# Kernel optimization log

Hardware: AMD Instinct MI355X
Metric: run time of the kernel (lower is better)

The kernel has to match this reference:

```python
import jax, jax.numpy as jnp
import numpy as np

HIDDEN = 768
NUM_HEADS = 8
NUM_CELLS = 16384
MAX_HDRS = 8
NUM_HEADERS = 512
LN_EPS = 1e-5


def setup_inputs() -> dict:
    key = jax.random.key(0)
    ks = jax.random.split(key, 16)
    s = 0.02
    D = HIDDEN
    return {
        "cell_value_embeddings": jax.random.normal(ks[0], (NUM_CELLS, D), jnp.float32),
        "header_embeddings": jax.random.normal(ks[1], (NUM_HEADERS, D), jnp.float32),
        "cell_to_header_map": jax.random.randint(ks[2], (NUM_CELLS, MAX_HDRS), 0, NUM_HEADERS),
        "cell_positions": jax.random.randint(ks[3], (NUM_CELLS, 2), 0, 100),
        # nn.MultiheadAttention params
        "in_proj_w": jax.random.normal(ks[4], (3 * D, D), jnp.float32) * s,
        "in_proj_b": jnp.zeros((3 * D,), jnp.float32),
        "out_w": jax.random.normal(ks[5], (D, D), jnp.float32) * s,
        "out_b": jnp.zeros((D,), jnp.float32),
        # positional embedding tables
        "row_emb": jax.random.normal(ks[6], (100, D), jnp.float32) * s,
        "col_emb": jax.random.normal(ks[7], (100, D), jnp.float32) * s,
        # fusion: Linear(2D->D) + LayerNorm
        "fus_w": jax.random.normal(ks[8], (D, 2 * D), jnp.float32) * s,
        "fus_b": jnp.zeros((D,), jnp.float32),
        "ln_g": jnp.ones((D,), jnp.float32),
        "ln_b": jnp.zeros((D,), jnp.float32),
    }


def _forward(cell_value_embeddings, header_embeddings, in_proj_w, in_proj_b,
             out_w, out_b, row_emb, col_emb, fus_w, fus_b, ln_g, ln_b,
             cell_to_header_map, cell_positions):
    N, D = cell_value_embeddings.shape
    H = cell_to_header_map.shape[1]
    nh, dh = NUM_HEADS, D // NUM_HEADS
    scale = 1.0 / (dh ** 0.5)

    pos = jnp.clip(cell_positions, 0, 99)
    cwp = cell_value_embeddings + row_emb[pos[:, 0]] + col_emb[pos[:, 1]]  # [N,D]

    ids = cell_to_header_map
    mask = ids >= 0                                   # [N,H] valid header slots
    hg = header_embeddings[jnp.where(mask, ids, 0)]   # [N,H,D] gathered K/V inputs

    Wq, Wk, Wv = jnp.split(in_proj_w, 3, axis=0)
    bq, bk, bv = jnp.split(in_proj_b, 3)
    q = (cwp @ Wq.T + bq).reshape(N, nh, dh)          # [N,a,d]
    k = (hg @ Wk.T + bk).reshape(N, H, nh, dh)        # [N,k,a,d]
    v = (hg @ Wv.T + bv).reshape(N, H, nh, dh)

    scores = jnp.einsum('nad,nkad->nak', q, k) * scale          # [N,a,k]
    scores = jnp.where(mask[:, None, :], scores, -1e9)
    attn = jax.nn.softmax(scores, axis=-1)
    attn = jnp.where(mask[:, None, :], attn, 0.0)
    ctx = jnp.einsum('nak,nkad->nad', attn, v).reshape(N, D)
    att_out = ctx @ out_w.T + out_b                    # [N,D]

    comb = jnp.concatenate([cwp, att_out], axis=-1)    # [N,2D]
    h = comb @ fus_w.T + fus_b
    mu = jnp.mean(h, axis=-1, keepdims=True)
    var = jnp.mean((h - mu) ** 2, axis=-1, keepdims=True)
    h = (h - mu) * jax.lax.rsqrt(var + LN_EPS) * ln_g + ln_b
    fused = jax.nn.relu(h)

    has = jnp.any(mask, axis=-1)                       # cells with >=1 valid header
    enriched = jnp.where(has[:, None], fused, cwp)
    weights = jnp.where(mask, attn.mean(axis=1), 0.0)  # head-averaged attn [N,H]
    return enriched, weights


def reference(cell_value_embeddings, header_embeddings, cell_to_header_map,
              cell_positions, in_proj_w, in_proj_b, out_w, out_b, row_emb,
              col_emb, fus_w, fus_b, ln_g, ln_b):
    return _forward(cell_value_embeddings, header_embeddings, in_proj_w,
                    in_proj_b, out_w, out_b, row_emb, col_emb, fus_w, fus_b,
                    ln_g, ln_b, cell_to_header_map, cell_positions)
```

## Files before the change

### kernel.cpp

```cpp
#include <hip/hip_runtime.h>
#include <hip/hip_bf16.h>

#define NCELLS 16384
#define DIM    768
#define NHEADS 8
#define DHEAD  96
#define MAXH   8
#define ND     (NCELLS * DIM)


using bf16 = __hip_bfloat16;
typedef short  short8  __attribute__((ext_vector_type(8)));
typedef short  short4v __attribute__((ext_vector_type(4)));
typedef float  floatx4 __attribute__((ext_vector_type(4)));

__device__ inline short f2b(float f) {
    bf16 h = __float2bfloat16(f);
    unsigned short u; __builtin_memcpy(&u, &h, 2); return (short)u;
}
__device__ inline float b2f(short u) {
    unsigned x = ((unsigned)(unsigned short)u) << 16;
    float f; __builtin_memcpy(&f, &x, 4); return f;
}

__device__ inline short8 ld8(const float* p) {
    floatx4 a = *reinterpret_cast<const floatx4*>(p);
    floatx4 b = *reinterpret_cast<const floatx4*>(p + 4);
    short8 o;
#pragma unroll
    for (int i = 0; i < 4; ++i) { o[i] = f2b(a[i]); o[i + 4] = f2b(b[i]); }
    return o;
}

__device__ __forceinline__ void cp16(const void* g, void* l) {
    __builtin_amdgcn_global_load_lds(
        (const __attribute__((address_space(1))) void*)g,
        (__attribute__((address_space(3))) void*)l, 16, 0, 0);
}

template <int DUAL, int COUT>
__global__ __launch_bounds__(256) void gemm_bf(
    const bf16* __restrict__ A, const bf16* __restrict__ A2,
    const bf16* __restrict__ W, int ldw,
    const float* __restrict__ bias,
    float* __restrict__ Cf, bf16* __restrict__ Cb, int K)
{
    __shared__ short As[128 * 64];
    __shared__ short Bs[128 * 64];
    const int tid = threadIdx.x, wave = tid >> 6, lane = tid & 63;
    const int id = blockIdx.x;
    const int m0 = (id & 127) * 128;
    const int n0 = (id >> 7) * 128;
    const int wr = (wave & 1) * 64, wc = (wave >> 1) * 64;
    const int fr = lane & 15, kg = lane >> 4;

    const int srow = lane >> 3;
    const int scol = (lane & 7) ^ srow;

    floatx4 acc[16];
#pragma unroll
    for (int i = 0; i < 16; ++i) acc[i] = (floatx4){0.f, 0.f, 0.f, 0.f};

    for (int k0 = 0; k0 < K; k0 += 64) {
        const bf16* Ak; int ka;
        if (!DUAL || k0 < DIM) { Ak = A;  ka = k0; }
        else                   { Ak = A2; ka = k0 - DIM; }

        __syncthreads();
#pragma unroll
        for (int i = 0; i < 4; ++i) {
            const int c = i * 4 + wave;
            const int row = c * 8 + srow;
            cp16(Ak + (size_t)(m0 + row) * DIM + ka + scol * 8,
                 &As[c * 512 + lane * 8]);
            cp16(W  + (size_t)(n0 + row) * ldw + k0 + scol * 8,
                 &Bs[c * 512 + lane * 8]);
        }
        __syncthreads();

#pragma unroll
        for (int kk = 0; kk < 2; ++kk) {
            short8 af[4], bfv[4];
#pragma unroll
            for (int i = 0; i < 4; ++i) {
                const int sa = ((kk * 4 + kg) ^ (fr & 7)) * 8;
                af[i]  = *reinterpret_cast<const short8*>(&As[(wr + i * 16 + fr) * 64 + sa]);
                bfv[i] = *reinterpret_cast<const short8*>(&Bs[(wc + i * 16 + fr) * 64 + sa]);
            }
#pragma unroll
            for (int i = 0; i < 4; ++i)
#pragma unroll
                for (int j = 0; j < 4; ++j)
                    acc[i * 4 + j] = __builtin_amdgcn_mfma_f32_16x16x32_bf16(
                        af[i], bfv[j], acc[i * 4 + j], 0, 0, 0);
        }
    }

    const int col_l = lane & 15, row_q = kg * 4;
#pragma unroll
    for (int j = 0; j < 4; ++j) {
        const int col = n0 + wc + j * 16 + col_l;
        const float bv = bias[col];
#pragma unroll
        for (int i = 0; i < 4; ++i) {
#pragma unroll
            for (int r = 0; r < 4; ++r) {
                const int row = m0 + wr + i * 16 + row_q + r;
                const float v = acc[i * 4 + j][r] + bv;
                if (COUT == 0) Cf[(size_t)row * DIM + col] = v;
                else           Cb[(size_t)row * DIM + col] = __float2bfloat16(v);
            }
        }
    }
}

__global__ __launch_bounds__(512) void gemm_ln_kernel(
    const bf16* __restrict__ A, const bf16* __restrict__ A2,
    const bf16* __restrict__ W,
    const float* __restrict__ bco, float* __restrict__ out,
    const int* __restrict__ map,
    const float* __restrict__ ce, const int* __restrict__ pos,
    const float* __restrict__ re, const float* __restrict__ co,
    const float* __restrict__ g, const float* __restrict__ b)
{
    __shared__ short As[8 * 512];
    __shared__ short Bs[32 * 512];
    __shared__ float rsum[64][4], rsq[64][4];
    __shared__ int   hasf[64];

    const int tid = threadIdx.x, wave = tid >> 6, lane = tid & 63;
    const int m0 = blockIdx.x * 64;
    const int wr = (wave & 1) * 32, wc = (wave >> 1) * 64;
    const int fr = lane & 15, kg = lane >> 4;
    const int srow = lane >> 3;
    const int scol = (lane & 7) ^ srow;
    const int col_l = lane & 15, rq = kg * 4;

    if (tid < 256) { ((float*)rsum)[tid] = 0.f; ((float*)rsq)[tid] = 0.f; }
    if (tid < 64) hasf[tid] = 0;

    for (int nt = 0; nt < 3; ++nt) {
        const int n0b = nt * 256;
        floatx4 acc[8];
#pragma unroll
        for (int i = 0; i < 8; ++i) acc[i] = (floatx4){0.f, 0.f, 0.f, 0.f};

        for (int k0 = 0; k0 < 1536; k0 += 64) {
            const bf16* Ak; int ka;
            if (k0 < DIM) { Ak = A;  ka = k0; }
            else          { Ak = A2; ka = k0 - DIM; }

            __syncthreads();
            cp16(Ak + (size_t)(m0 + wave * 8 + srow) * DIM + ka + scol * 8,
                 &As[wave * 512 + lane * 8]);
#pragma unroll
            for (int u = 0; u < 4; ++u) {
                const int c2 = wave * 4 + u;
                cp16(W + (size_t)(n0b + c2 * 8 + srow) * 1536 + k0 + scol * 8,
                     &Bs[c2 * 512 + lane * 8]);
            }
            __syncthreads();

#pragma unroll
            for (int kk = 0; kk < 2; ++kk) {
                const int sa = ((kk * 4 + kg) ^ (fr & 7)) * 8;
                short8 af[2], bv[4];
#pragma unroll
                for (int i = 0; i < 2; ++i)
                    af[i] = *reinterpret_cast<const short8*>(&As[(wr + i * 16 + fr) * 64 + sa]);
#pragma unroll
                for (int j = 0; j < 4; ++j)
                    bv[j] = *reinterpret_cast<const short8*>(&Bs[(wc + j * 16 + fr) * 64 + sa]);
#pragma unroll
                for (int i = 0; i < 2; ++i)
#pragma unroll
                    for (int j = 0; j < 4; ++j)
                        acc[i * 4 + j] = __builtin_amdgcn_mfma_f32_16x16x32_bf16(
                            af[i], bv[j], acc[i * 4 + j], 0, 0, 0);
            }
        }

        float bcov[4];
#pragma unroll
        for (int j = 0; j < 4; ++j) bcov[j] = bco[n0b + wc + j * 16 + col_l];
#pragma unroll
        for (int i = 0; i < 2; ++i) {
#pragma unroll
            for (int r = 0; r < 4; ++r) {
                const int rowl = wr + i * 16 + rq + r;
                float s = 0.f, q = 0.f;
#pragma unroll
                for (int j = 0; j < 4; ++j) {
                    const int col = n0b + wc + j * 16 + col_l;
                    const float v = acc[i * 4 + j][r] + bcov[j];
                    out[(size_t)(m0 + rowl) * DIM + col] = v;
                    s += v; q += v * v;
                }
#pragma unroll
                for (int off = 1; off < 16; off <<= 1) {
                    s += __shfl_xor(s, off);
                    q += __shfl_xor(q, off);
                }
                if (col_l == 0) {
                    rsum[rowl][wave >> 1] += s;
                    rsq[rowl][wave >> 1]  += q;
                }
            }
        }
    }

    {
        const int row = tid >> 3, sl = tid & 7;
        if (map[(size_t)(m0 + row) * MAXH + sl] >= 0) hasf[row] = 1;
    }
    __syncthreads();

    {
        const int rowl = tid >> 3, c0 = (tid & 7) * 96;
        const int grow = m0 + rowl;
        const float sr = rsum[rowl][0] + rsum[rowl][1] + rsum[rowl][2] + rsum[rowl][3];
        const float qr = rsq[rowl][0] + rsq[rowl][1] + rsq[rowl][2] + rsq[rowl][3];
        const float mu  = sr * (1.f / 768.f);
        const float var = qr * (1.f / 768.f) - mu * mu;
        const float inv = rsqrtf(var + 1e-5f);
        float* hp = out + (size_t)grow * DIM + c0;

        if (hasf[rowl]) {
#pragma unroll 4
            for (int bq = 0; bq < 24; ++bq) {
                floatx4 hv = *reinterpret_cast<const floatx4*>(hp + bq * 4);
                floatx4 gv = *reinterpret_cast<const floatx4*>(g + c0 + bq * 4);
                floatx4 bv = *reinterpret_cast<const floatx4*>(b + c0 + bq * 4);
                floatx4 o;
#pragma unroll
                for (int e = 0; e < 4; ++e)
                    o[e] = fmaxf((hv[e] - mu) * inv * gv[e] + bv[e], 0.f);
                *reinterpret_cast<floatx4*>(hp + bq * 4) = o;
            }
        } else {
            int pr = pos[grow * 2 + 0]; pr = min(max(pr, 0), 99);
            int pc = pos[grow * 2 + 1]; pc = min(max(pc, 0), 99);
#pragma unroll 4
            for (int bq = 0; bq < 24; ++bq) {
                floatx4 a0 = *reinterpret_cast<const floatx4*>(ce + (size_t)grow * DIM + c0 + bq * 4);
                floatx4 b0 = *reinterpret_cast<const floatx4*>(re + (size_t)pr * DIM + c0 + bq * 4);
                floatx4 c1 = *reinterpret_cast<const floatx4*>(co + (size_t)pc * DIM + c0 + bq * 4);
                floatx4 o;
#pragma unroll
                for (int e = 0; e < 4; ++e) o[e] = a0[e] + b0[e] + c1[e];
                *reinterpret_cast<floatx4*>(hp + bq * 4) = o;
            }
        }
    }
}

__global__ __launch_bounds__(256) void prep_kernel(
    const float* __restrict__ ce, const int* __restrict__ pos,
    const float* __restrict__ re, const float* __restrict__ co,
    bf16* __restrict__ cwp_b,
    const float* __restrict__ in_proj_w, bf16* __restrict__ Wq_b,
    const float* __restrict__ fus_w,     bf16* __restrict__ Wf_b,
    const float* __restrict__ out_w, const float* __restrict__ out_b,
    const float* __restrict__ fus_b, float* __restrict__ bco,
    const float* __restrict__ hdr, const float* __restrict__ in_proj_b,
    bf16* __restrict__ HKV)
{
    __shared__ short As[64 * 72];
    __shared__ short Bs[64 * 72];
    const int b = blockIdx.x, tid = threadIdx.x;

    if (b < 192) {
        const int m0 = (b & 7) * 64, n0 = (b >> 3) * 64;
        const float* W = in_proj_w + (size_t)DIM * DIM;
        const float* bias = in_proj_b + DIM;
        const int wave = tid >> 6, lane = tid & 63;
        const int lr = tid >> 2, lc = (tid & 3) * 16;
        const int fr = lane & 15, fk = (lane >> 4) * 8;

        floatx4 acc[4];
#pragma unroll
        for (int i = 0; i < 4; ++i) acc[i] = (floatx4){0.f, 0.f, 0.f, 0.f};

        const float* ap = hdr + (size_t)(m0 + lr) * DIM + lc;
        const float* wp = W   + (size_t)(n0 + lr) * DIM + lc;
        short8 a0 = ld8(ap), a1 = ld8(ap + 8);
        short8 w0 = ld8(wp), w1 = ld8(wp + 8);

        for (int it = 0; it < 12; ++it) {
            __syncthreads();
            *reinterpret_cast<short8*>(&As[lr * 72 + lc])     = a0;
            *reinterpret_cast<short8*>(&As[lr * 72 + lc + 8]) = a1;
            *reinterpret_cast<short8*>(&Bs[lr * 72 + lc])     = w0;
            *reinterpret_cast<short8*>(&Bs[lr * 72 + lc + 8]) = w1;
            __syncthreads();
            if (it < 11) {
                const int k0 = (it + 1) * 64;
                a0 = ld8(ap + k0); a1 = ld8(ap + k0 + 8);
                w0 = ld8(wp + k0); w1 = ld8(wp + k0 + 8);
            }
#pragma unroll
            for (int kk = 0; kk < 2; ++kk) {
                short8 af = *reinterpret_cast<const short8*>(
                    &As[(wave * 16 + fr) * 72 + kk * 32 + fk]);
#pragma unroll
                for (int t = 0; t < 4; ++t) {
                    short8 bfv = *reinterpret_cast<const short8*>(
                        &Bs[(t * 16 + fr) * 72 + kk * 32 + fk]);
                    acc[t] = __builtin_amdgcn_mfma_f32_16x16x32_bf16(af, bfv, acc[t], 0, 0, 0);
                }
            }
        }
        const int col_l = lane & 15, row_q = (lane >> 4) * 4;
#pragma unroll
        for (int t = 0; t < 4; ++t) {
            const int col = n0 + t * 16 + col_l;
            const float bv = bias[col];
#pragma unroll
            for (int r = 0; r < 4; ++r) {
                const int row = m0 + wave * 16 + row_q + r;
                HKV[(size_t)row * 1536 + col] = __float2bfloat16(acc[t][r] + bv);
            }
        }
    } else if (b < 336) {
        const int b3 = b - 192;
        const int n0  = (b3 % 12) * 64;
        const int k0t = (b3 / 12) * 64;
        const int wave = tid >> 6, lane = tid & 63;
        const int lr = tid >> 2, lc = (tid & 3) * 16;
        const int fr = lane & 15, fk = (lane >> 4) * 8;

        floatx4 acc[4];
#pragma unroll
        for (int i = 0; i < 4; ++i) acc[i] = (floatx4){0.f, 0.f, 0.f, 0.f};

        const float* ap = fus_w + (size_t)(n0 + lr) * 1536 + 768 + lc;
        const float* bp = out_w + (size_t)lr * DIM + k0t + lc;
        short8 a0 = ld8(ap), a1 = ld8(ap + 8);
        floatx4 q0 = *reinterpret_cast<const floatx4*>(bp);
        floatx4 q1 = *reinterpret_cast<const floatx4*>(bp + 4);
        floatx4 q2 = *reinterpret_cast<const floatx4*>(bp + 8);
        floatx4 q3 = *reinterpret_cast<const floatx4*>(bp + 12);

        for (int it = 0; it < 12; ++it) {
            __syncthreads();
            *reinterpret_cast<short8*>(&As[lr * 72 + lc])     = a0;
            *reinterpret_cast<short8*>(&As[lr * 72 + lc + 8]) = a1;
#pragma unroll
            for (int e = 0; e < 4; ++e) {
                Bs[(lc + e) * 72 + lr]      = f2b(q0[e]);
                Bs[(lc + 4 + e) * 72 + lr]  = f2b(q1[e]);
                Bs[(lc + 8 + e) * 72 + lr]  = f2b(q2[e]);
                Bs[(lc + 12 + e) * 72 + lr] = f2b(q3[e]);
            }
            __syncthreads();
            if (it < 11) {
                const int r0 = (it + 1) * 64;
                a0 = ld8(ap + r0); a1 = ld8(ap + r0 + 8);
                const float* bq = bp + (size_t)r0 * DIM;
                q0 = *reinterpret_cast<const floatx4*>(bq);
                q1 = *reinterpret_cast<const floatx4*>(bq + 4);
                q2 = *reinterpret_cast<const floatx4*>(bq + 8);
                q3 = *reinterpret_cast<const floatx4*>(bq + 12);
            }
#pragma unroll
            for (int kk = 0; kk < 2; ++kk) {
                short8 af = *reinterpret_cast<const short8*>(
                    &As[(wave * 16 + fr) * 72 + kk * 32 + fk]);
#pragma unroll
                for (int t = 0; t < 4; ++t) {
                    short8 bfv = *reinterpret_cast<const short8*>(
                        &Bs[(t * 16 + fr) * 72 + kk * 32 + fk]);
                    acc[t] = __builtin_amdgcn_mfma_f32_16x16x32_bf16(af, bfv, acc[t], 0, 0, 0);
                }
            }
        }
        const int col_l = lane & 15, row_q = (lane >> 4) * 4;
#pragma unroll
        for (int t = 0; t < 4; ++t) {
            const int col = k0t + t * 16 + col_l;
#pragma unroll
            for (int r = 0; r < 4; ++r) {
                const int row = n0 + wave * 16 + row_q + r;
                Wf_b[(size_t)row * 1536 + 768 + col] = __float2bfloat16(acc[t][r]);
            }
        }
    } else if (b < 339) {
        const int n = (b - 336) * 256 + tid;
        const float* wrow = fus_w + (size_t)n * 1536 + 768;
        float acc = fus_b[n];
#pragma unroll 4
        for (int m = 0; m < 768; m += 4) {
            floatx4 wv = *reinterpret_cast<const floatx4*>(wrow + m);
            floatx4 ob = *reinterpret_cast<const floatx4*>(out_b + m);
            acc += wv[0] * ob[0] + wv[1] * ob[1] + wv[2] * ob[2] + wv[3] * ob[3];
        }
        bco[n] = acc;
    } else if (b < 915) {
        const int i = (b - 339) * 256 + tid;
        floatx4 v = *reinterpret_cast<const floatx4*>(in_proj_w + (size_t)i * 4);
        short4v o;
#pragma unroll
        for (int j = 0; j < 4; ++j) o[j] = f2b(v[j]);
        *reinterpret_cast<short4v*>((short*)Wq_b + (size_t)i * 4) = o;
    } else if (b < 1491) {
        const int i  = (b - 915) * 256 + tid;
        const int e0 = i * 4;
        const int n  = e0 / 768;
        const int k  = e0 - n * 768;
        const size_t src = (size_t)n * 1536 + k;
        floatx4 v = *reinterpret_cast<const floatx4*>(fus_w + src);
        short4v o;
#pragma unroll
        for (int j = 0; j < 4; ++j) o[j] = f2b(v[j]);
        *reinterpret_cast<short4v*>((short*)Wf_b + src) = o;
    } else {
        const int gid  = (b - 1491) * 256 + tid;
        const int cell = gid / 96;
        const int off  = (gid % 96) * 8;
        int pr = pos[cell * 2 + 0]; pr = min(max(pr, 0), 99);
        int pc = pos[cell * 2 + 1]; pc = min(max(pc, 0), 99);
        const float* a = ce + (size_t)cell * DIM + off;
        const float* bb = re + (size_t)pr * DIM + off;
        const float* c = co + (size_t)pc * DIM + off;
        floatx4 a0 = *reinterpret_cast<const floatx4*>(a);
        floatx4 a1 = *reinterpret_cast<const floatx4*>(a + 4);
        floatx4 b0 = *reinterpret_cast<const floatx4*>(bb);
        floatx4 b1 = *reinterpret_cast<const floatx4*>(bb + 4);
        floatx4 c0 = *reinterpret_cast<const floatx4*>(c);
        floatx4 c1 = *reinterpret_cast<const floatx4*>(c + 4);
        short8 o;
#pragma unroll
        for (int i = 0; i < 4; ++i) {
            o[i]     = f2b(a0[i] + b0[i] + c0[i]);
            o[i + 4] = f2b(a1[i] + b1[i] + c1[i]);
        }
        *reinterpret_cast<short8*>((short*)cwp_b + (size_t)cell * DIM + off) = o;
    }
}

__global__ __launch_bounds__(256) void attn_l_kernel(
    const bf16* __restrict__ q, bf16* __restrict__ ctx,
    const bf16* __restrict__ HKV, const int* __restrict__ map,
    float* __restrict__ wout)
{
    const int h = threadIdx.x >> 7;
    const int t = threadIdx.x & 127;
    const int cell = blockIdx.x * 2 + h;

    __shared__ short Ks[2][8 * 768];
    __shared__ int   ids[2][MAXH];
    __shared__ float msk[2][MAXH];
    __shared__ float at_l[2][64];

    if (t < MAXH) {
        int id = map[(size_t)cell * MAXH + t];
        msk[h][t] = (id >= 0) ? 1.f : 0.f;
        ids[h][t] = (id >= 0) ? id : 0;
    }

    const int a = t >> 3, j = t & 7;
    short8 qv[12];
    if (t < 64) {
        const short* qp = (const short*)q + (size_t)cell * DIM + a * DHEAD;
#pragma unroll
        for (int c = 0; c < 12; ++c)
            qv[c] = *reinterpret_cast<const short8*>(qp + c * 8);
    }

#pragma unroll
    for (int s = 0; s < 6; ++s) {
        const int P  = s * 128 + t;
        const int jr = P / 96;
        const int gi = (P - jr * 96) ^ (jr & 7);
        int id = map[(size_t)cell * MAXH + jr];
        id = (id >= 0) ? id : 0;
        cp16((const short*)HKV + (size_t)id * 1536 + gi * 8, &Ks[h][P * 8]);
    }
    __syncthreads();

    short8 vv[8];
    if (t < 96) {
        const int d0 = t * 8;
#pragma unroll
        for (int jj = 0; jj < 8; ++jj)
            vv[jj] = *reinterpret_cast<const short8*>(
                (const short*)HKV + (size_t)ids[h][jj] * 1536 + DIM + d0);
    }

    if (t < 64) {
        float s0 = 0.f, s1 = 0.f, s2 = 0.f, s3 = 0.f;
#pragma unroll
        for (int cc = 0; cc < 12; cc += 4) {
            short8 kv[4];
#pragma unroll
            for (int u = 0; u < 4; ++u) {
                const int gi = (a * 12 + cc + u) ^ (j & 7);
                kv[u] = *reinterpret_cast<const short8*>(&Ks[h][(j * 96 + gi) * 8]);
            }
#pragma unroll
            for (int e = 0; e < 8; ++e) {
                s0 += b2f(qv[cc    ][e]) * b2f(kv[0][e]);
                s1 += b2f(qv[cc + 1][e]) * b2f(kv[1][e]);
                s2 += b2f(qv[cc + 2][e]) * b2f(kv[2][e]);
                s3 += b2f(qv[cc + 3][e]) * b2f(kv[3][e]);
            }
        }
        float s = ((s0 + s1) + (s2 + s3)) * 0.10206207261596577f;
        const float mk = msk[h][j];
        s = (mk != 0.f) ? s : -1e9f;
        float m = s;
        m = fmaxf(m, __shfl_xor(m, 1));
        m = fmaxf(m, __shfl_xor(m, 2));
        m = fmaxf(m, __shfl_xor(m, 4));
        float e = expf(s - m) * mk;
        float sum = e;
        sum += __shfl_xor(sum, 1);
        sum += __shfl_xor(sum, 2);
        sum += __shfl_xor(sum, 4);
        at_l[h][t] = (sum > 0.f) ? e / sum : 0.f;
    }
    __syncthreads();

    if (t < 96) {
        const int d0 = t * 8, ha = t / 12;
        float w[8];
#pragma unroll
        for (int jj = 0; jj < 8; ++jj) w[jj] = at_l[h][ha * 8 + jj];
        float acc[8];
#pragma unroll
        for (int e = 0; e < 8; ++e) acc[e] = 0.f;
#pragma unroll
        for (int jj = 0; jj < 8; ++jj)
#pragma unroll
            for (int e = 0; e < 8; ++e) acc[e] += w[jj] * b2f(vv[jj][e]);
        short8 o;
#pragma unroll
        for (int e = 0; e < 8; ++e) o[e] = f2b(acc[e]);
        *reinterpret_cast<short8*>((short*)ctx + (size_t)cell * DIM + d0) = o;
    } else if (t < 96 + MAXH) {
        const int jj = t - 96;
        float s = 0.f;
#pragma unroll
        for (int a2 = 0; a2 < NHEADS; ++a2) s += at_l[h][a2 * 8 + jj];
        wout[(size_t)cell * MAXH + jj] = s * 0.125f;
    }
}

extern "C" void kernel_launch(void* const* d_in, const int* in_sizes, int n_in,
                              void* d_out, int out_size, void* d_ws, size_t ws_size,
                              hipStream_t stream) {
    (void)in_sizes; (void)n_in; (void)out_size; (void)ws_size;

    const float* cell_emb  = (const float*)d_in[0];
    const float* hdr_emb   = (const float*)d_in[1];
    const int*   map       = (const int*)d_in[2];
    const int*   pos       = (const int*)d_in[3];
    const float* in_proj_w = (const float*)d_in[4];
    const float* in_proj_b = (const float*)d_in[5];
    const float* out_w     = (const float*)d_in[6];
    const float* out_b     = (const float*)d_in[7];
    const float* row_emb   = (const float*)d_in[8];
    const float* col_emb   = (const float*)d_in[9];
    const float* fus_w     = (const float*)d_in[10];
    const float* fus_b     = (const float*)d_in[11];
    const float* ln_g      = (const float*)d_in[12];
    const float* ln_b      = (const float*)d_in[13];
    float* out = (float*)d_out;

    char* ws = (char*)d_ws;
    bf16*  HKV   = (bf16*)ws;
    bf16*  ctx_b = (bf16*)(ws + 1572864);
    bf16*  cwp_b = (bf16*)(ws + 26738688);
    bf16*  Wq_b  = (bf16*)(ws + 51904512);
    float* bco   = (float*)(ws + 53084160);
    bf16*  Wf_b  = (bf16*)(ws + 54263808);
    bf16* q_b = (bf16*)d_out;

    prep_kernel<<<7635, 256, 0, stream>>>(
        cell_emb, pos, row_emb, col_emb, cwp_b,
        in_proj_w, Wq_b, fus_w, Wf_b,
        out_w, out_b, fus_b, bco,
        hdr_emb, in_proj_b, HKV);

    gemm_bf<0, 1><<<768, 256, 0, stream>>>(
        cwp_b, nullptr, Wq_b, DIM, in_proj_b, nullptr, q_b, DIM);

    attn_l_kernel<<<NCELLS / 2, 256, 0, stream>>>(q_b, ctx_b, HKV, map, out + ND);

    gemm_ln_kernel<<<256, 512, 0, stream>>>(
        cwp_b, ctx_b, Wf_b, bco, out, map,
        cell_emb, pos, row_emb, col_emb, ln_g, ln_b);
}
```

Measured before the change: 334.8 us.

## Split fusion GEMM across N tiles with grid-wide barrier for LayerNorm stats

Replaces the 256-block fusion GEMM+LayerNorm kernel, where each block computed full 768-wide rows in three sequential N passes, with 768 blocks of 128x128 tiles. Per-row partial sums are written to a global scratch buffer, a grid-wide atomic counter barrier waits for all blocks, and then each block normalizes its own tile from registers. This raises parallelism and avoids writing and re-reading the pre-norm output. The barrier relies on all 768 blocks being co-resident (launch_bounds 256,3), and risks a deadlock or spin cost if they are not. The scratch buffer reuses the Wq_b workspace region.

```diff
diff --git a/kernel.cpp b/kernel.cpp
--- a/kernel.cpp
+++ b/kernel.cpp
@@ -114,141 +114,165 @@
     }
 }
 
-__global__ __launch_bounds__(512) void gemm_ln_kernel(
+__global__ __launch_bounds__(256, 3) void fusion_ln_sync(
     const bf16* __restrict__ A, const bf16* __restrict__ A2,
     const bf16* __restrict__ W,
-    const float* __restrict__ bco, float* __restrict__ out,
+    const float* __restrict__ bias, float* __restrict__ out,
+    float* __restrict__ Sg,
+    int* __restrict__ ctr,
     const int* __restrict__ map,
     const float* __restrict__ ce, const int* __restrict__ pos,
     const float* __restrict__ re, const float* __restrict__ co,
     const float* __restrict__ g, const float* __restrict__ b)
 {
-    __shared__ short As[8 * 512];
-    __shared__ short Bs[32 * 512];
-    __shared__ float rsum[64][4], rsq[64][4];
-    __shared__ int   hasf[64];
+    __shared__ short As[128 * 64];
+    __shared__ short Bs[128 * 64];
+    __shared__ float rs[128][2], rq2[128][2];
+    __shared__ float muL[128], invL[128];
+    __shared__ int   hasL[128];
 
     const int tid = threadIdx.x, wave = tid >> 6, lane = tid & 63;
-    const int m0 = blockIdx.x * 64;
-    const int wr = (wave & 1) * 32, wc = (wave >> 1) * 64;
+    const int id = blockIdx.x;
+    const int mt = id & 127, nt = id >> 7;
+    const int m0 = mt * 128, n0 = nt * 128;
+    const int wr = (wave & 1) * 64, wc = (wave >> 1) * 64;
     const int fr = lane & 15, kg = lane >> 4;
     const int srow = lane >> 3;
     const int scol = (lane & 7) ^ srow;
-    const int col_l = lane & 15, rq = kg * 4;
-
-    if (tid < 256) { ((float*)rsum)[tid] = 0.f; ((float*)rsq)[tid] = 0.f; }
-    if (tid < 64) hasf[tid] = 0;
-
-    for (int nt = 0; nt < 3; ++nt) {
-        const int n0b = nt * 256;
-        floatx4 acc[8];
-#pragma unroll
-        for (int i = 0; i < 8; ++i) acc[i] = (floatx4){0.f, 0.f, 0.f, 0.f};
-
-        for (int k0 = 0; k0 < 1536; k0 += 64) {
-            const bf16* Ak; int ka;
-            if (k0 < DIM) { Ak = A;  ka = k0; }
-            else          { Ak = A2; ka = k0 - DIM; }
-
-            __syncthreads();
-            cp16(Ak + (size_t)(m0 + wave * 8 + srow) * DIM + ka + scol * 8,
-                 &As[wave * 512 + lane * 8]);
-#pragma unroll
-            for (int u = 0; u < 4; ++u) {
-                const int c2 = wave * 4 + u;
-                cp16(W + (size_t)(n0b + c2 * 8 + srow) * 1536 + k0 + scol * 8,
-                     &Bs[c2 * 512 + lane * 8]);
-            }
-            __syncthreads();
-
-#pragma unroll
-            for (int kk = 0; kk < 2; ++kk) {
+
+    floatx4 acc[16];
+#pragma unroll
+    for (int i = 0; i < 16; ++i) acc[i] = (floatx4){0.f, 0.f, 0.f, 0.f};
+
+    for (int k0 = 0; k0 < 1536; k0 += 64) {
+        const bf16* Ak; int ka;
+        if (k0 < DIM) { Ak = A;  ka = k0; }
+        else          { Ak = A2; ka = k0 - DIM; }
+
+        __syncthreads();
+#pragma unroll
+        for (int i = 0; i < 4; ++i) {
+            const int c = i * 4 + wave;
+            const int row = c * 8 + srow;
+            cp16(Ak + (size_t)(m0 + row) * DIM + ka + scol * 8,
+                 &As[c * 512 + lane * 8]);
+            cp16(W  + (size_t)(n0 + row) * 1536 + k0 + scol * 8,
+                 &Bs[c * 512 + lane * 8]);
+        }
+        __syncthreads();
+
+#pragma unroll
+        for (int kk = 0; kk < 2; ++kk) {
+            short8 af[4], bfv[4];
+#pragma unroll
+            for (int i = 0; i < 4; ++i) {
                 const int sa = ((kk * 4 + kg) ^ (fr & 7)) * 8;
-                short8 af[2], bv[4];
-#pragma unroll
-                for (int i = 0; i < 2; ++i)
-                    af[i] = *reinterpret_cast<const short8*>(&As[(wr + i * 16 + fr) * 64 + sa]);
+                af[i]  = *reinterpret_cast<const short8*>(&As[(wr + i * 16 + fr) * 64 + sa]);
+                bfv[i] = *reinterpret_cast<const short8*>(&Bs[(wc + i * 16 + fr) * 64 + sa]);
+            }
+#pragma unroll
+            for (int i = 0; i < 4; ++i)
 #pragma unroll
                 for (int j = 0; j < 4; ++j)
-                    bv[j] = *reinterpret_cast<const short8*>(&Bs[(wc + j * 16 + fr) * 64 + sa]);
-#pragma unroll
-                for (int i = 0; i < 2; ++i)
-#pragma unroll
-                    for (int j = 0; j < 4; ++j)
-                        acc[i * 4 + j] = __builtin_amdgcn_mfma_f32_16x16x32_bf16(
-                            af[i], bv[j], acc[i * 4 + j], 0, 0, 0);
-            }
-        }
-
-        float bcov[4];
-#pragma unroll
-        for (int j = 0; j < 4; ++j) bcov[j] = bco[n0b + wc + j * 16 + col_l];
-#pragma unroll
-        for (int i = 0; i < 2; ++i) {
-#pragma unroll
-            for (int r = 0; r < 4; ++r) {
-                const int rowl = wr + i * 16 + rq + r;
-                float s = 0.f, q = 0.f;
+                    acc[i * 4 + j] = __builtin_amdgcn_mfma_f32_16x16x32_bf16(
+                        af[i], bfv[j], acc[i * 4 + j], 0, 0, 0);
+        }
+    }
+
+    const int col_l = lane & 15, row_q = kg * 4;
+    float bcov[4], gv4[4], bv4[4];
+#pragma unroll
+    for (int j = 0; j < 4; ++j) {
+        const int col = n0 + wc + j * 16 + col_l;
+        bcov[j] = bias[col]; gv4[j] = g[col]; bv4[j] = b[col];
+    }
+#pragma unroll
+    for (int i = 0; i < 4; ++i)
+#pragma unroll
+        for (int j = 0; j < 4; ++j)
+#pragma unroll
+            for (int r = 0; r < 4; ++r)
+                acc[i * 4 + j][r] += bcov[j];
+
+#pragma unroll
+    for (int i = 0; i < 4; ++i) {
+#pragma unroll
+        for (int r = 0; r < 4; ++r) {
+            const int rowl = wr + i * 16 + row_q + r;
+            float s = 0.f, q = 0.f;
+#pragma unroll
+            for (int j = 0; j < 4; ++j) {
+                const float v = acc[i * 4 + j][r];
+                s += v; q += v * v;
+            }
+#pragma unroll
+            for (int off = 1; off < 16; off <<= 1) {
+                s += __shfl_xor(s, off);
+                q += __shfl_xor(q, off);
+            }
+            if (col_l == 0) { rs[rowl][wc >> 6] = s; rq2[rowl][wc >> 6] = q; }
+        }
+    }
+    __syncthreads();
+    if (tid < 128) {
+        const float s = rs[tid][0] + rs[tid][1];
+        const float q = rq2[tid][0] + rq2[tid][1];
+        float2* Sp = (float2*)Sg + ((size_t)mt * 128 + tid) * 6 + nt;
+        *Sp = make_float2(s, q);
+    }
+
+    __syncthreads();
+    __threadfence();
+    if (tid == 0) {
+        __hip_atomic_fetch_add(ctr, 1, __ATOMIC_ACQ_REL, __HIP_MEMORY_SCOPE_AGENT);
+        while (__hip_atomic_load(ctr, __ATOMIC_ACQUIRE, __HIP_MEMORY_SCOPE_AGENT)
+               < (int)gridDim.x) { __builtin_amdgcn_s_sleep(8); }
+    }
+    __syncthreads();
+
+    if (tid < 128) {
+        const float2* Sp = (const float2*)Sg + ((size_t)mt * 128 + tid) * 6;
+        float s = 0.f, q = 0.f;
+#pragma unroll
+        for (int k = 0; k < 6; ++k) { float2 v = Sp[k]; s += v.x; q += v.y; }
+        const float mu  = s * (1.f / 768.f);
+        const float var = q * (1.f / 768.f) - mu * mu;
+        muL[tid]  = mu;
+        invL[tid] = rsqrtf(var + 1e-5f);
+        int hb = 0;
+#pragma unroll
+        for (int sl = 0; sl < MAXH; ++sl)
+            if (map[(size_t)(m0 + tid) * MAXH + sl] >= 0) hb = 1;
+        hasL[tid] = hb;
+    }
+    __syncthreads();
+
+#pragma unroll
+    for (int i = 0; i < 4; ++i) {
+#pragma unroll
+        for (int r = 0; r < 4; ++r) {
+            const int rowl = wr + i * 16 + row_q + r;
+            const int grow = m0 + rowl;
+            if (hasL[rowl]) {
+                const float mu = muL[rowl], inv = invL[rowl];
 #pragma unroll
                 for (int j = 0; j < 4; ++j) {
-                    const int col = n0b + wc + j * 16 + col_l;
-                    const float v = acc[i * 4 + j][r] + bcov[j];
-                    out[(size_t)(m0 + rowl) * DIM + col] = v;
-                    s += v; q += v * v;
+                    const int col = n0 + wc + j * 16 + col_l;
+                    const float v = acc[i * 4 + j][r];
+                    out[(size_t)grow * DIM + col] =
+                        fmaxf((v - mu) * inv * gv4[j] + bv4[j], 0.f);
                 }
-#pragma unroll
-                for (int off = 1; off < 16; off <<= 1) {
-                    s += __shfl_xor(s, off);
-                    q += __shfl_xor(q, off);
+            } else {
+                int pr = pos[grow * 2 + 0]; pr = min(max(pr, 0), 99);
+                int pc = pos[grow * 2 + 1]; pc = min(max(pc, 0), 99);
+#pragma unroll
+                for (int j = 0; j < 4; ++j) {
+                    const int col = n0 + wc + j * 16 + col_l;
+                    out[(size_t)grow * DIM + col] =
+                        ce[(size_t)grow * DIM + col] +
+                        re[(size_t)pr * DIM + col] +
+                        co[(size_t)pc * DIM + col];
                 }
-                if (col_l == 0) {
-                    rsum[rowl][wave >> 1] += s;
-                    rsq[rowl][wave >> 1]  += q;
-                }
-            }
-        }
-    }
-
-    {
-        const int row = tid >> 3, sl = tid & 7;
-        if (map[(size_t)(m0 + row) * MAXH + sl] >= 0) hasf[row] = 1;
-    }
-    __syncthreads();
-
-    {
-        const int rowl = tid >> 3, c0 = (tid & 7) * 96;
-        const int grow = m0 + rowl;
-        const float sr = rsum[rowl][0] + rsum[rowl][1] + rsum[rowl][2] + rsum[rowl][3];
-        const float qr = rsq[rowl][0] + rsq[rowl][1] + rsq[rowl][2] + rsq[rowl][3];
-        const float mu  = sr * (1.f / 768.f);
-        const float var = qr * (1.f / 768.f) - mu * mu;
-        const float inv = rsqrtf(var + 1e-5f);
-        float* hp = out + (size_t)grow * DIM + c0;
-
-        if (hasf[rowl]) {
-#pragma unroll 4
-            for (int bq = 0; bq < 24; ++bq) {
-                floatx4 hv = *reinterpret_cast<const floatx4*>(hp + bq * 4);
-                floatx4 gv = *reinterpret_cast<const floatx4*>(g + c0 + bq * 4);
-                floatx4 bv = *reinterpret_cast<const floatx4*>(b + c0 + bq * 4);
-                floatx4 o;
-#pragma unroll
-                for (int e = 0; e < 4; ++e)
-                    o[e] = fmaxf((hv[e] - mu) * inv * gv[e] + bv[e], 0.f);
-                *reinterpret_cast<floatx4*>(hp + bq * 4) = o;
-            }
-        } else {
-            int pr = pos[grow * 2 + 0]; pr = min(max(pr, 0), 99);
-            int pc = pos[grow * 2 + 1]; pc = min(max(pc, 0), 99);
-#pragma unroll 4
-            for (int bq = 0; bq < 24; ++bq) {
-                floatx4 a0 = *reinterpret_cast<const floatx4*>(ce + (size_t)grow * DIM + c0 + bq * 4);
-                floatx4 b0 = *reinterpret_cast<const floatx4*>(re + (size_t)pr * DIM + c0 + bq * 4);
-                floatx4 c1 = *reinterpret_cast<const floatx4*>(co + (size_t)pc * DIM + c0 + bq * 4);
-                floatx4 o;
-#pragma unroll
-                for (int e = 0; e < 4; ++e) o[e] = a0[e] + b0[e] + c1[e];
-                *reinterpret_cast<floatx4*>(hp + bq * 4) = o;
             }
         }
     }
@@ -263,7 +287,7 @@
     const float* __restrict__ out_w, const float* __restrict__ out_b,
     const float* __restrict__ fus_b, float* __restrict__ bco,
     const float* __restrict__ hdr, const float* __restrict__ in_proj_b,
-    bf16* __restrict__ HKV)
+    bf16* __restrict__ HKV, int* __restrict__ ctr)
 {
     __shared__ short As[64 * 72];
     __shared__ short Bs[64 * 72];
@@ -385,6 +409,7 @@
             }
         }
     } else if (b < 339) {
+        if (b == 336 && tid == 0) *ctr = 0;
         const int n = (b - 336) * 256 + tid;
         const float* wrow = fus_w + (size_t)n * 1536 + 768;
         float acc = fus_b[n];
@@ -572,7 +597,9 @@
     bf16*  ctx_b = (bf16*)(ws + 1572864);
     bf16*  cwp_b = (bf16*)(ws + 26738688);
     bf16*  Wq_b  = (bf16*)(ws + 51904512);
+    float* Sg    = (float*)(ws + 51904512);
     float* bco   = (float*)(ws + 53084160);
+    int*   ctr   = (int*)(ws + 53087232);
     bf16*  Wf_b  = (bf16*)(ws + 54263808);
     bf16* q_b = (bf16*)d_out;
 
@@ -580,14 +607,14 @@
         cell_emb, pos, row_emb, col_emb, cwp_b,
         in_proj_w, Wq_b, fus_w, Wf_b,
         out_w, out_b, fus_b, bco,
-        hdr_emb, in_proj_b, HKV);
+        hdr_emb, in_proj_b, HKV, ctr);
 
     gemm_bf<0, 1><<<768, 256, 0, stream>>>(
         cwp_b, nullptr, Wq_b, DIM, in_proj_b, nullptr, q_b, DIM);
 
     attn_l_kernel<<<NCELLS / 2, 256, 0, stream>>>(q_b, ctx_b, HKV, map, out + ND);
 
-    gemm_ln_kernel<<<256, 512, 0, stream>>>(
-        cwp_b, ctx_b, Wf_b, bco, out, map,
+    fusion_ln_sync<<<768, 256, 0, stream>>>(
+        cwp_b, ctx_b, Wf_b, bco, out, Sg, ctr, map,
         cell_emb, pos, row_emb, col_emb, ln_g, ln_b);
 }
```

Measured after the change: 353.3 us. +5.5%, slower.
